# Kernel tuning notes

Measured on AMD Instinct MI355X. Metric: run time of the kernel, lower is better.

The kernel has to match this reference:

```python
import jax, jax.numpy as jnp
import numpy as np

B, L, E, H = 2, 2048, 1024, 16
D = E // H  # 64


def setup_inputs() -> dict:
    key = jax.random.key(0)
    ks = jax.random.split(key, 9)
    return {
        "query": jax.random.normal(ks[0], (B, L, E), dtype=jnp.float32),
        "value": jax.random.normal(ks[1], (B, L, E), dtype=jnp.float32),
        "key": jax.random.normal(ks[2], (B, L, E), dtype=jnp.float32),
        "mask": jax.random.randint(ks[3], (B, 1, L, L), 0, 2, dtype=jnp.int32),
        "Wq": jax.random.normal(ks[4], (D, D), dtype=jnp.float32) * 0.05,
        "Wk": jax.random.normal(ks[5], (D, D), dtype=jnp.float32) * 0.05,
        "Wv": jax.random.normal(ks[6], (D, D), dtype=jnp.float32) * 0.05,
        "Wfc": jax.random.normal(ks[7], (E, E), dtype=jnp.float32) * 0.02,
        "bfc": jax.random.normal(ks[8], (E,), dtype=jnp.float32) * 0.02,
    }


def reference(query, value, key, mask, Wq, Wk, Wv, Wfc, bfc):
    b, q_len, _ = query.shape
    k_len = key.shape[1]
    v_len = value.shape[1]
    # split heads: [b, l, H, D]
    q = query.reshape(b, q_len, H, D)
    k = key.reshape(b, k_len, H, D)
    v = value.reshape(b, v_len, H, D)
    # per-head linear projections (shared weights across heads, no bias)
    q = jnp.einsum('bqhd,ed->bqhe', q, Wq)
    k = jnp.einsum('bkhd,ed->bkhe', k, Wk)
    v = jnp.einsum('bvhd,ed->bvhe', v, Wv)
    # attention scores [b, H, q, k]
    attn = jnp.einsum('bqhd,bkhd->bhqk', q, k)
    # NOTE: original masks BEFORE scaling, and scales by sqrt(embedding_size)
    attn = jnp.where(mask == 0, jnp.float32(-1e20), attn)
    attn = attn / jnp.float32(E ** 0.5)
    attn = jax.nn.softmax(attn, axis=3)
    out = jnp.einsum('bhqk,bkhd->bqhd', attn, v).reshape(b, q_len, E)
    out = out @ Wfc.T + bfc
    return out
```

## Files before the change

kernel.cpp:

```cpp
#include <hip/hip_runtime.h>
#include <hip/hip_bf16.h>


#define B_ 2
#define L_ 2048
#define E_ 1024
#define H_ 16
#define D_ 64

typedef __attribute__((ext_vector_type(8))) short s8v;
typedef __attribute__((ext_vector_type(4))) float f4v;
typedef __attribute__((ext_vector_type(2))) float f2v;

__device__ __forceinline__ f4v mfma16(s8v a, s8v b, f4v c) {
    return __builtin_amdgcn_mfma_f32_16x16x32_bf16(a, b, c, 0, 0, 0);
}

__device__ __forceinline__ float fast_exp2(float x) {
    return __builtin_amdgcn_exp2f(x);
}

__device__ __forceinline__ ushort bf16bits(float f) {
    __hip_bfloat16 h = __float2bfloat16(f);
    return *(ushort*)&h;
}

__device__ __forceinline__ void glds16(const __hip_bfloat16* g, ushort* l) {
    __builtin_amdgcn_global_load_lds(
        (const __attribute__((address_space(1))) void*)g,
        (__attribute__((address_space(3))) void*)l,
        16, 0, 0);
}

__device__ __forceinline__ s8v ld8_dual(const void* p, size_t idx, bool isf32) {
    if (isf32) {
        const float* pf = (const float*)p + idx;
        f4v f0 = *(const f4v*)pf;
        f4v f1 = *(const f4v*)(pf + 4);
        s8v r;
        r[0] = (short)bf16bits(f0[0]); r[1] = (short)bf16bits(f0[1]);
        r[2] = (short)bf16bits(f0[2]); r[3] = (short)bf16bits(f0[3]);
        r[4] = (short)bf16bits(f1[0]); r[5] = (short)bf16bits(f1[1]);
        r[6] = (short)bf16bits(f1[2]); r[7] = (short)bf16bits(f1[3]);
        return r;
    }
    return *(const s8v*)((const __hip_bfloat16*)p + idx);
}

__device__ __forceinline__ s8v ld8_ws(const __hip_bfloat16* p) {
    return *(const s8v*)p;
}

__device__ __forceinline__ s8v u4_to_s8(uint a, uint b, uint c, uint d) {
    union { uint u[4]; s8v v; } x;
    x.u[0] = a; x.u[1] = b; x.u[2] = c; x.u[3] = d;
    return x.v;
}

__device__ __forceinline__ bool block_detect_f32(const void* q_in, int* sflag) {
    if (threadIdx.x == 0) *sflag = 0;
    __syncthreads();
    const ushort* qq = (const ushort*)q_in + (threadIdx.x & 255) * 16;
    int bad = 0;
    #pragma unroll
    for (int i = 0; i < 16; ++i) bad += (((qq[i] >> 7) & 0xFF) >= 0x8E);
    bad += __shfl_xor(bad, 1);
    bad += __shfl_xor(bad, 2);
    bad += __shfl_xor(bad, 4);
    bad += __shfl_xor(bad, 8);
    bad += __shfl_xor(bad, 16);
    bad += __shfl_xor(bad, 32);
    if ((threadIdx.x & 63) == 0 && threadIdx.x < 256) atomicAdd(sflag, bad);
    __syncthreads();
    return *sflag > 100;
}

__device__ __forceinline__ void cvt_piece(
    size_t i4, const void* Wfc, const void* bfc,
    __hip_bfloat16* wfc_bf, __hip_bfloat16* bfc_bf, bool isf32)
{
    const size_t base = i4 * 4;
    const size_t n1 = (size_t)E_ * E_;
    if (base >= n1 + E_) return;
    const void* src = (base < n1) ? Wfc : bfc;
    const size_t off = (base < n1) ? base : base - n1;
    __hip_bfloat16* dst = (base < n1) ? (wfc_bf + off) : (bfc_bf + off);
    if (isf32) {
        f4v v = *(const f4v*)((const float*)src + off);
        #pragma unroll
        for (int j = 0; j < 4; ++j) dst[j] = __float2bfloat16(v[j]);
    } else {
        *(ushort4*)dst = *(const ushort4*)((const ushort*)src + off);
    }
}

__global__ __launch_bounds__(256) void proj_all_kernel(
    const void* __restrict__ q_in, const void* __restrict__ k_in,
    const void* __restrict__ v_in,
    const void* __restrict__ Wq, const void* __restrict__ Wk,
    const void* __restrict__ Wv,
    const void* __restrict__ Wfc, const void* __restrict__ bfc,
    const int* __restrict__ mask, unsigned long long* __restrict__ mbits,
    __hip_bfloat16* __restrict__ qp, __hip_bfloat16* __restrict__ kp,
    __hip_bfloat16* __restrict__ vpT,
    __hip_bfloat16* __restrict__ wfc_bf, __hip_bfloat16* __restrict__ bfc_bf)
{
    __shared__ __align__(16) ushort tile[64][72];
    __shared__ __align__(16) ushort wlds[64 * 72];
    __shared__ int sflag;
    const int wave = threadIdx.x >> 6;
    const int lane = threadIdx.x & 63;
    const int quad = lane >> 4;
    const int l16  = lane & 15;

    if (blockIdx.y == 3) {
        const int lane_ = threadIdx.x & 63;
        const size_t wbase = (size_t)blockIdx.x * 128 + wave * 32;
        #pragma unroll 4
        for (int i = 0; i < 32; ++i) {
            const size_t widx = wbase + i;
            const int v = mask[widx * 64 + lane_];
            const unsigned long long bal = __ballot(v != 0);
            if (lane_ == 0) mbits[widx] = bal;
        }
        return;
    }

    const bool isf32 = block_detect_f32(q_in, &sflag);

    if (blockIdx.y == 4) {
        cvt_piece((size_t)blockIdx.x * 256 + threadIdx.x, Wfc, bfc, wfc_bf, bfc_bf, isf32);
        if (blockIdx.x == 0)
            cvt_piece((size_t)(E_ * (size_t)E_ / 4) + threadIdx.x, Wfc, bfc, wfc_bf, bfc_bf, isf32);
        return;
    }

    {
        const void* W = blockIdx.y == 0 ? Wq : (blockIdx.y == 1 ? Wk : Wv);
        const int row = threadIdx.x >> 2;
        const int c0  = (threadIdx.x & 3) * 16;
        if (isf32) {
            const float* wsrc = (const float*)W + row * 64 + c0;
            #pragma unroll
            for (int j = 0; j < 16; ++j)
                wlds[row * 72 + c0 + j] = bf16bits(wsrc[j]);
        } else {
            const ushort* wsrc = (const ushort*)W + row * 64 + c0;
            *(s8v*)&wlds[row * 72 + c0]     = *(const s8v*)wsrc;
            *(s8v*)&wlds[row * 72 + c0 + 8] = *(const s8v*)(wsrc + 8);
        }
    }
    __syncthreads();

    if (blockIdx.y < 2) {
        const void* X = blockIdx.y == 0 ? q_in : k_in;
        __hip_bfloat16* dst = blockIdx.y == 0 ? qp : kp;
        const float oscale = (blockIdx.y == 0) ? 0.045084439755930314f : 1.0f;
        const int m0 = (blockIdx.x * 4 + wave) * 16;

        const size_t abase = (size_t)(m0 + l16) * D_;
        s8v a0 = ld8_dual(X, abase + quad * 8, isf32);
        s8v a1 = ld8_dual(X, abase + 32 + quad * 8, isf32);

        f4v acc[4];
        #pragma unroll
        for (int nt = 0; nt < 4; ++nt) {
            const ushort* wr = &wlds[(nt * 16 + l16) * 72];
            s8v b0 = *(const s8v*)(wr + quad * 8);
            s8v b1 = *(const s8v*)(wr + 32 + quad * 8);
            f4v c = {0.f, 0.f, 0.f, 0.f};
            c = mfma16(a0, b0, c);
            c = mfma16(a1, b1, c);
            acc[nt] = c;
        }
        #pragma unroll
        for (int r = 0; r < 4; ++r) {
            const int m = m0 + quad * 4 + r;
            const int h = m & 15;
            const int bl = m >> 4;
            const int b = bl >> 11;
            const int l = bl & (L_ - 1);
            #pragma unroll
            for (int nt = 0; nt < 4; ++nt) {
                const int e = nt * 16 + l16;
                dst[(((size_t)(b * H_ + h)) * L_ + l) * D_ + e] =
                    __float2bfloat16(acc[nt][r] * oscale);
            }
        }
    } else {
        const int l0 = (blockIdx.x & 31) * 64;
        const int bh = blockIdx.x >> 5;
        const int b = bh >> 4, h = bh & 15;
        const int lw = l0 + wave * 16;

        const size_t xbase = ((size_t)(b * L_ + lw + l16)) * E_ + h * D_;
        s8v a0 = ld8_dual(v_in, xbase + quad * 8, isf32);
        s8v a1 = ld8_dual(v_in, xbase + 32 + quad * 8, isf32);

        #pragma unroll
        for (int nt = 0; nt < 4; ++nt) {
            const int e = nt * 16 + l16;
            const ushort* wr = &wlds[e * 72];
            s8v b0 = *(const s8v*)(wr + quad * 8);
            s8v b1 = *(const s8v*)(wr + 32 + quad * 8);
            f4v c = {0.f, 0.f, 0.f, 0.f};
            c = mfma16(a0, b0, c);
            c = mfma16(a1, b1, c);
            #pragma unroll
            for (int r = 0; r < 4; ++r)
                tile[wave * 16 + quad * 4 + r][e] = bf16bits(c[r]);
        }
        __syncthreads();
        const int e  = threadIdx.x >> 2;
        const int lc = (threadIdx.x & 3) * 16;
        s8v s0, s1;
        #pragma unroll
        for (int i = 0; i < 8; ++i) {
            s0[i] = (short)tile[lc + i][e];
            s1[i] = (short)tile[lc + 8 + i][e];
        }
        __hip_bfloat16* drow = vpT + ((size_t)bh * D_ + e) * L_ + l0 + lc;
        *(s8v*)drow = s0;
        *(s8v*)(drow + 8) = s1;
    }
}

__global__ __launch_bounds__(256) void cvt_wfc_kernel(
    const void* __restrict__ Wfc, const void* __restrict__ bfc,
    __hip_bfloat16* __restrict__ wfc_bf, __hip_bfloat16* __restrict__ bfc_bf,
    const void* __restrict__ q_in)
{
    __shared__ int sflag;
    const bool isf32 = block_detect_f32(q_in, &sflag);
    cvt_piece((size_t)blockIdx.x * 256 + threadIdx.x, Wfc, bfc, wfc_bf, bfc_bf, isf32);
}

__global__ __launch_bounds__(256, 2) void attn_kernel(
    const __hip_bfloat16* __restrict__ qp,
    const __hip_bfloat16* __restrict__ kp,
    const __hip_bfloat16* __restrict__ vpT,
    const unsigned long long* __restrict__ mbits,
    __hip_bfloat16* __restrict__ attn_out)
{
    __shared__ __align__(16) ushort kv[4][2][64 * 64];

    const int wave = threadIdx.x >> 6;
    const int lane = threadIdx.x & 63;
    const int quad = lane >> 4;
    const int l16  = lane & 15;
    const int sw   = l16 & 7;
    const int bh = blockIdx.y;
    const int b = bh >> 4, h = bh & 15;
    const int q0 = blockIdx.x * 128 + wave * 32;

    const __hip_bfloat16* kbh = kp + (size_t)bh * L_ * D_;
    const __hip_bfloat16* vbh = vpT + (size_t)bh * D_ * L_;
    const unsigned long long* mrowA = mbits + ((size_t)b * L_ + q0 + l16) * 32;
    const unsigned long long* mrowB = mrowA + 16 * 32;

    const int lrow = lane >> 3;
    const int lchk = (lane & 7) ^ lrow;
    const int r0 = wave * 16;
    const __hip_bfloat16* kg0 = kbh + (size_t)(r0 + lrow) * D_ + lchk * 8;
    const __hip_bfloat16* kg1 = kbh + (size_t)(r0 + 8 + lrow) * D_ + lchk * 8;
    const __hip_bfloat16* vg0 = vbh + (size_t)(r0 + lrow) * L_ + lchk * 8;
    const __hip_bfloat16* vg1 = vbh + (size_t)(r0 + 8 + lrow) * L_ + lchk * 8;

    const __hip_bfloat16* qbase = qp + ((size_t)bh * L_ + q0) * D_;
    s8v qaA0 = ld8_ws(qbase + (size_t)l16 * D_ + quad * 8);
    s8v qaA1 = ld8_ws(qbase + (size_t)l16 * D_ + 32 + quad * 8);
    s8v qaB0 = ld8_ws(qbase + (size_t)(16 + l16) * D_ + quad * 8);
    s8v qaB1 = ld8_ws(qbase + (size_t)(16 + l16) * D_ + 32 + quad * 8);

    f2v rs2A = {0.f, 0.f}, rs2B = {0.f, 0.f};
    f4v oA[4], oB[4];
    #pragma unroll
    for (int nt = 0; nt < 4; ++nt) {
        oA[nt] = (f4v){0.f, 0.f, 0.f, 0.f};
        oB[nt] = (f4v){0.f, 0.f, 0.f, 0.f};
    }

    const int ro0 = l16 * 64 + ((quad ^ sw) << 3);
    const int ro1 = l16 * 64 + (((quad + 4) ^ sw) << 3);
    const int shq = quad * 4;

    unsigned long long wqA0 = 0, wqA1 = 0, wqA2 = 0, wqA3 = 0;
    unsigned long long wqB0 = 0, wqB1 = 0, wqB2 = 0, wqB3 = 0;

    glds16(kg0, &kv[0][0][r0 * 64]);
    glds16(kg1, &kv[0][0][r0 * 64 + 512]);
    glds16(vg0, &kv[0][1][r0 * 64]);
    glds16(vg1, &kv[0][1][r0 * 64 + 512]);
    wqA0 = mrowA[0]; wqB0 = mrowB[0];
    kg0 += 64 * D_; kg1 += 64 * D_; vg0 += 64; vg1 += 64;
    glds16(kg0, &kv[1][0][r0 * 64]);
    glds16(kg1, &kv[1][0][r0 * 64 + 512]);
    glds16(vg0, &kv[1][1][r0 * 64]);
    glds16(vg1, &kv[1][1][r0 * 64 + 512]);
    wqA1 = mrowA[1]; wqB1 = mrowB[1];
    kg0 += 64 * D_; kg1 += 64 * D_; vg0 += 64; vg1 += 64;

#define SM_T(SARR_, WLO_, WHI_, RS_, PA0_, PA1_)                               \
    {                                                                          \
        uint dw[4][2];                                                         \
        _Pragma("unroll")                                                      \
        for (int nt = 0; nt < 4; ++nt) {                                       \
            const uint hs = (nt & 2) ? WHI_ : WLO_;                            \
            float pr[4];                                                       \
            _Pragma("unroll")                                                  \
            for (int r = 0; r < 4; ++r) {                                      \
                const float p = fast_exp2(SARR_[nt][r]);                       \
                const int m = __builtin_amdgcn_sbfe((int)hs,                   \
                                  ((nt & 1) << 4) + r, 1);                     \
                pr[r] = __uint_as_float(__float_as_uint(p) & (uint)m);         \
            }                                                                  \
            RS_ += (f2v){pr[0], pr[1]};                                        \
            RS_ += (f2v){pr[2], pr[3]};                                        \
            asm("v_cvt_pk_bf16_f32 %0, %1, %2"                                 \
                : "=v"(dw[nt][0]) : "v"(pr[0]), "v"(pr[1]));                   \
            asm("v_cvt_pk_bf16_f32 %0, %1, %2"                                 \
                : "=v"(dw[nt][1]) : "v"(pr[2]), "v"(pr[3]));                   \
        }                                                                      \
        uint w00 = dw[0][0], w10 = dw[1][0];                                   \
        uint w01 = dw[0][1], w11 = dw[1][1];                                   \
        uint w20 = dw[2][0], w30 = dw[3][0];                                   \
        uint w21 = dw[2][1], w31 = dw[3][1];                                   \
        asm("v_permlane32_swap_b32 %0, %1" : "+v"(w00), "+v"(w10));            \
        asm("v_permlane16_swap_b32 %0, %1" : "+v"(w00), "+v"(w10));            \
        asm("v_permlane32_swap_b32 %0, %1" : "+v"(w01), "+v"(w11));            \
        asm("v_permlane16_swap_b32 %0, %1" : "+v"(w01), "+v"(w11));            \
        asm("v_permlane32_swap_b32 %0, %1" : "+v"(w20), "+v"(w30));            \
        asm("v_permlane16_swap_b32 %0, %1" : "+v"(w20), "+v"(w30));            \
        asm("v_permlane32_swap_b32 %0, %1" : "+v"(w21), "+v"(w31));            \
        asm("v_permlane16_swap_b32 %0, %1" : "+v"(w21), "+v"(w31));            \
        PA0_ = u4_to_s8(w00, w01, w10, w11);                                   \
        PA1_ = u4_to_s8(w20, w21, w30, w31);                                   \
    }

#define ATTN_BODY(IT_, CUR_, DST_, PRE_, VMASM_)                               \
    {                                                                          \
        if (PRE_) {                                                            \
            glds16(kg0, &kv[DST_][0][r0 * 64]);                                \
            glds16(kg1, &kv[DST_][0][r0 * 64 + 512]);                          \
            glds16(vg0, &kv[DST_][1][r0 * 64]);                                \
            glds16(vg1, &kv[DST_][1][r0 * 64 + 512]);                          \
            wqA##DST_ = mrowA[(IT_) + 2];                                      \
            wqB##DST_ = mrowB[(IT_) + 2];                                      \
            kg0 += 64 * D_; kg1 += 64 * D_; vg0 += 64; vg1 += 64;              \
        }                                                                      \
        asm volatile(VMASM_ ::: "memory");                                     \
        __builtin_amdgcn_s_barrier();                                          \
        __builtin_amdgcn_sched_barrier(0);                                     \
        const uint wloA = ((uint)wqA##CUR_) >> shq;                            \
        const uint whiA = ((uint)(wqA##CUR_ >> 32)) >> shq;                    \
        const uint wloB = ((uint)wqB##CUR_) >> shq;                            \
        const uint whiB = ((uint)(wqB##CUR_ >> 32)) >> shq;                    \
        f4v sA[4], sB[4];                                                      \
        __builtin_amdgcn_s_setprio(1);                                         \
        _Pragma("unroll")                                                      \
        for (int nt = 0; nt < 4; ++nt) {                                       \
            s8v kb0 = *(const s8v*)&kv[CUR_][0][nt * 1024 + ro0];              \
            s8v kb1 = *(const s8v*)&kv[CUR_][0][nt * 1024 + ro1];              \
            f4v cA = {0.f, 0.f, 0.f, 0.f};                                     \
            f4v cB = {0.f, 0.f, 0.f, 0.f};                                     \
            cA = mfma16(kb0, qaA0, cA);                                        \
            cA = mfma16(kb1, qaA1, cA);                                        \
            cB = mfma16(kb0, qaB0, cB);                                        \
            cB = mfma16(kb1, qaB1, cB);                                        \
            sA[nt] = cA; sB[nt] = cB;                                          \
        }                                                                      \
        __builtin_amdgcn_s_setprio(0);                                         \
        s8v paA0, paA1, paB0, paB1;                                            \
        SM_T(sA, wloA, whiA, rs2A, paA0, paA1)                                 \
        SM_T(sB, wloB, whiB, rs2B, paB0, paB1)                                 \
        __builtin_amdgcn_s_setprio(1);                                         \
        _Pragma("unroll")                                                      \
        for (int nt = 0; nt < 4; ++nt) {                                       \
            s8v vb0 = *(const s8v*)&kv[CUR_][1][nt * 1024 + ro0];              \
            s8v vb1 = *(const s8v*)&kv[CUR_][1][nt * 1024 + ro1];              \
            oA[nt] = mfma16(paA0, vb0, oA[nt]);                                \
            oA[nt] = mfma16(paA1, vb1, oA[nt]);                                \
            oB[nt] = mfma16(paB0, vb0, oB[nt]);                                \
            oB[nt] = mfma16(paB1, vb1, oB[nt]);                                \
        }                                                                      \
        __builtin_amdgcn_s_setprio(0);                                         \
    }

    for (int it4 = 0; it4 < 7; ++it4) {
        const int t = it4 * 4;
        ATTN_BODY(t,     0, 2, true, "s_waitcnt vmcnt(12)")
        ATTN_BODY(t + 1, 1, 3, true, "s_waitcnt vmcnt(12)")
        ATTN_BODY(t + 2, 2, 0, true, "s_waitcnt vmcnt(12)")
        ATTN_BODY(t + 3, 3, 1, true, "s_waitcnt vmcnt(12)")
    }
    ATTN_BODY(28, 0, 2, true,  "s_waitcnt vmcnt(12)")
    ATTN_BODY(29, 1, 3, true,  "s_waitcnt vmcnt(12)")
    ATTN_BODY(30, 2, 0, false, "s_waitcnt vmcnt(6)")
    ATTN_BODY(31, 3, 1, false, "s_waitcnt vmcnt(0)")
#undef ATTN_BODY
#undef SM_T

    float vA = rs2A[0] + rs2A[1];
    vA += __shfl_xor(vA, 16, 64);
    vA += __shfl_xor(vA, 32, 64);
    float vB = rs2B[0] + rs2B[1];
    vB += __shfl_xor(vB, 16, 64);
    vB += __shfl_xor(vB, 32, 64);
    #pragma unroll
    for (int r = 0; r < 4; ++r) {
        const int qrow = quad * 4 + r;
        const float liA = __shfl(vA, qrow, 64);
        const float invA = 1.0f / fmaxf(liA, 1e-30f);
        const float liB = __shfl(vB, qrow, 64);
        const float invB = 1.0f / fmaxf(liB, 1e-30f);
        const int rowA = q0 + qrow;
        const int rowB = q0 + 16 + qrow;
        #pragma unroll
        for (int nt = 0; nt < 4; ++nt) {
            const int d = nt * 16 + l16;
            attn_out[((size_t)(b * L_ + rowA)) * E_ + h * D_ + d] =
                __float2bfloat16(oA[nt][r] * invA);
            attn_out[((size_t)(b * L_ + rowB)) * E_ + h * D_ + d] =
                __float2bfloat16(oB[nt][r] * invB);
        }
    }
}

__global__ __launch_bounds__(256, 4) void fc_kernel(
    const __hip_bfloat16* __restrict__ x,
    const __hip_bfloat16* __restrict__ wfc_bf,
    const __hip_bfloat16* __restrict__ bfc_bf,
    void* __restrict__ out, const void* __restrict__ q_in)
{
    __shared__ __align__(16) ushort abuf[2][128 * 64];
    __shared__ __align__(16) ushort bbuf[2][64 * 64];
    __shared__ int sflag;
    const bool isf32 = block_detect_f32(q_in, &sflag);
    const int wave = threadIdx.x >> 6;
    const int lane = threadIdx.x & 63;
    const int quad = lane >> 4;
    const int l16  = lane & 15;
    const int sw   = l16 & 7;
    const int m0 = blockIdx.x * 128;
    const int n0 = blockIdx.y * 64;
    const int wr = wave >> 1;
    const int wc = wave & 1;

    const int lrow = lane >> 3;
    const int lchk = (lane & 7) ^ lrow;

    const __hip_bfloat16* ag[4];
    #pragma unroll
    for (int c = 0; c < 4; ++c)
        ag[c] = x + (size_t)(m0 + c * 32 + wave * 8 + lrow) * E_ + lchk * 8;
    const __hip_bfloat16* bg[2];
    #pragma unroll
    for (int c = 0; c < 2; ++c)
        bg[c] = wfc_bf + (size_t)(n0 + c * 32 + wave * 8 + lrow) * E_ + lchk * 8;

    f4v acc[4][2];
    #pragma unroll
    for (int fm = 0; fm < 4; ++fm)
        #pragma unroll
        for (int fn = 0; fn < 2; ++fn) acc[fm][fn] = (f4v){0.f, 0.f, 0.f, 0.f};

    #pragma unroll
    for (int c = 0; c < 4; ++c) glds16(ag[c], &abuf[0][(c * 32 + wave * 8) * 64]);
    #pragma unroll
    for (int c = 0; c < 2; ++c) glds16(bg[c], &bbuf[0][(c * 32 + wave * 8) * 64]);
    __syncthreads();

    int cur = 0;
    for (int it = 0; it < 16; ++it) {
        if (it < 15) {
            #pragma unroll
            for (int c = 0; c < 4; ++c)
                glds16(ag[c] + (it + 1) * 64, &abuf[cur ^ 1][(c * 32 + wave * 8) * 64]);
            #pragma unroll
            for (int c = 0; c < 2; ++c)
                glds16(bg[c] + (it + 1) * 64, &bbuf[cur ^ 1][(c * 32 + wave * 8) * 64]);
        }
        s8v a0[4], a1[4];
        #pragma unroll
        for (int fm = 0; fm < 4; ++fm) {
            const ushort* ar = &abuf[cur][(wr * 64 + fm * 16 + l16) * 64];
            a0[fm] = *(const s8v*)(ar + ((quad ^ sw) << 3));
            a1[fm] = *(const s8v*)(ar + (((quad + 4) ^ sw) << 3));
        }
        #pragma unroll
        for (int fn = 0; fn < 2; ++fn) {
            const ushort* br = &bbuf[cur][(wc * 32 + fn * 16 + l16) * 64];
            s8v b0 = *(const s8v*)(br + ((quad ^ sw) << 3));
            s8v b1 = *(const s8v*)(br + (((quad + 4) ^ sw) << 3));
            #pragma unroll
            for (int fm = 0; fm < 4; ++fm) {
                acc[fm][fn] = mfma16(a0[fm], b0, acc[fm][fn]);
                acc[fm][fn] = mfma16(a1[fm], b1, acc[fm][fn]);
            }
        }
        __syncthreads();
        cur ^= 1;
    }
    #pragma unroll
    for (int fm = 0; fm < 4; ++fm) {
        #pragma unroll
        for (int r = 0; r < 4; ++r) {
            const int m = m0 + wr * 64 + fm * 16 + quad * 4 + r;
            #pragma unroll
            for (int fn = 0; fn < 2; ++fn) {
                const int n = n0 + wc * 32 + fn * 16 + l16;
                const float val = acc[fm][fn][r] + __bfloat162float(bfc_bf[n]);
                if (isf32) ((float*)out)[(size_t)m * E_ + n] = val;
                else       ((__hip_bfloat16*)out)[(size_t)m * E_ + n] = __float2bfloat16(val);
            }
        }
    }
}

extern "C" void kernel_launch(void* const* d_in, const int* in_sizes, int n_in,
                              void* d_out, int out_size, void* d_ws, size_t ws_size,
                              hipStream_t stream) {
    const void* query = d_in[0];
    const void* value = d_in[1];
    const void* key   = d_in[2];
    const int*  mask  = (const int*)d_in[3];
    const void* Wq  = d_in[4];
    const void* Wk  = d_in[5];
    const void* Wv  = d_in[6];
    const void* Wfc = d_in[7];
    const void* bfc = d_in[8];

    char* ws = (char*)d_ws;
    unsigned long long* mbits     = (unsigned long long*)(ws + (64u << 10));
    __hip_bfloat16* qp            = (__hip_bfloat16*)(ws + (2u  << 20));
    __hip_bfloat16* kp            = (__hip_bfloat16*)(ws + (10u << 20));
    __hip_bfloat16* vpT           = (__hip_bfloat16*)(ws + (18u << 20));
    __hip_bfloat16* attn_out      = (__hip_bfloat16*)(ws + (26u << 20));

    const bool big_ws = ws_size >= (37ull << 20);
    __hip_bfloat16* wfc_bf = big_ws ? (__hip_bfloat16*)(ws + (34ull << 20)) : qp;
    __hip_bfloat16* bfc_bf = wfc_bf + (size_t)E_ * E_;

    proj_all_kernel<<<dim3(1024, big_ws ? 5 : 4), 256, 0, stream>>>(
        query, key, value, Wq, Wk, Wv, Wfc, bfc, mask, mbits,
        qp, kp, vpT, wfc_bf, bfc_bf);
    attn_kernel<<<dim3(16, 32), 256, 0, stream>>>(qp, kp, vpT, mbits, attn_out);
    if (!big_ws)
        cvt_wfc_kernel<<<1025, 256, 0, stream>>>(Wfc, bfc, wfc_bf, bfc_bf, query);
    fc_kernel<<<dim3(32, 16), 256, 0, stream>>>(attn_out, wfc_bf, bfc_bf, d_out, query);
}
```

Before: 221.0 us.

## Double attention workgroup to 8 waves sharing each K/V LDS tile

Each attention workgroup now runs 8 waves covering 256 query rows instead of 4 waves covering 128, with half as many blocks. Every wave loads 8 rows of each K/V tile instead of 16, so each staged tile is reused by twice as many query rows and global K/V traffic per query row halves. The vmcnt wait thresholds drop to match the smaller per-wave load count. The trade-offs are more waves waiting at each barrier and a grid of 256 blocks, which may underfill the GPU's compute units.

```diff
diff --git a/kernel.cpp b/kernel.cpp
--- a/kernel.cpp
+++ b/kernel.cpp
@@ -235,7 +235,7 @@
     cvt_piece((size_t)blockIdx.x * 256 + threadIdx.x, Wfc, bfc, wfc_bf, bfc_bf, isf32);
 }
 
-__global__ __launch_bounds__(256, 2) void attn_kernel(
+__global__ __launch_bounds__(512, 2) void attn_kernel(
     const __hip_bfloat16* __restrict__ qp,
     const __hip_bfloat16* __restrict__ kp,
     const __hip_bfloat16* __restrict__ vpT,
@@ -251,7 +251,7 @@
     const int sw   = l16 & 7;
     const int bh = blockIdx.y;
     const int b = bh >> 4, h = bh & 15;
-    const int q0 = blockIdx.x * 128 + wave * 32;
+    const int q0 = blockIdx.x * 256 + wave * 32;
 
     const __hip_bfloat16* kbh = kp + (size_t)bh * L_ * D_;
     const __hip_bfloat16* vbh = vpT + (size_t)bh * D_ * L_;
@@ -260,11 +260,9 @@
 
     const int lrow = lane >> 3;
     const int lchk = (lane & 7) ^ lrow;
-    const int r0 = wave * 16;
-    const __hip_bfloat16* kg0 = kbh + (size_t)(r0 + lrow) * D_ + lchk * 8;
-    const __hip_bfloat16* kg1 = kbh + (size_t)(r0 + 8 + lrow) * D_ + lchk * 8;
-    const __hip_bfloat16* vg0 = vbh + (size_t)(r0 + lrow) * L_ + lchk * 8;
-    const __hip_bfloat16* vg1 = vbh + (size_t)(r0 + 8 + lrow) * L_ + lchk * 8;
+    const int r0 = wave * 8;
+    const __hip_bfloat16* kg = kbh + (size_t)(r0 + lrow) * D_ + lchk * 8;
+    const __hip_bfloat16* vg = vbh + (size_t)(r0 + lrow) * L_ + lchk * 8;
 
     const __hip_bfloat16* qbase = qp + ((size_t)bh * L_ + q0) * D_;
     s8v qaA0 = ld8_ws(qbase + (size_t)l16 * D_ + quad * 8);
@@ -287,18 +285,14 @@
     unsigned long long wqA0 = 0, wqA1 = 0, wqA2 = 0, wqA3 = 0;
     unsigned long long wqB0 = 0, wqB1 = 0, wqB2 = 0, wqB3 = 0;
 
-    glds16(kg0, &kv[0][0][r0 * 64]);
-    glds16(kg1, &kv[0][0][r0 * 64 + 512]);
-    glds16(vg0, &kv[0][1][r0 * 64]);
-    glds16(vg1, &kv[0][1][r0 * 64 + 512]);
+    glds16(kg, &kv[0][0][r0 * 64]);
+    glds16(vg, &kv[0][1][r0 * 64]);
     wqA0 = mrowA[0]; wqB0 = mrowB[0];
-    kg0 += 64 * D_; kg1 += 64 * D_; vg0 += 64; vg1 += 64;
-    glds16(kg0, &kv[1][0][r0 * 64]);
-    glds16(kg1, &kv[1][0][r0 * 64 + 512]);
-    glds16(vg0, &kv[1][1][r0 * 64]);
-    glds16(vg1, &kv[1][1][r0 * 64 + 512]);
+    kg += 64 * D_; vg += 64;
+    glds16(kg, &kv[1][0][r0 * 64]);
+    glds16(vg, &kv[1][1][r0 * 64]);
     wqA1 = mrowA[1]; wqB1 = mrowB[1];
-    kg0 += 64 * D_; kg1 += 64 * D_; vg0 += 64; vg1 += 64;
+    kg += 64 * D_; vg += 64;
 
 #define SM_T(SARR_, WLO_, WHI_, RS_, PA0_, PA1_)                               \
     {                                                                          \
@@ -340,13 +334,11 @@
 #define ATTN_BODY(IT_, CUR_, DST_, PRE_, VMASM_)                               \
     {                                                                          \
         if (PRE_) {                                                            \
-            glds16(kg0, &kv[DST_][0][r0 * 64]);                                \
-            glds16(kg1, &kv[DST_][0][r0 * 64 + 512]);                          \
-            glds16(vg0, &kv[DST_][1][r0 * 64]);                                \
-            glds16(vg1, &kv[DST_][1][r0 * 64 + 512]);                          \
+            glds16(kg, &kv[DST_][0][r0 * 64]);                                 \
+            glds16(vg, &kv[DST_][1][r0 * 64]);                                 \
             wqA##DST_ = mrowA[(IT_) + 2];                                      \
             wqB##DST_ = mrowB[(IT_) + 2];                                      \
-            kg0 += 64 * D_; kg1 += 64 * D_; vg0 += 64; vg1 += 64;              \
+            kg += 64 * D_; vg += 64;                                           \
         }                                                                      \
         asm volatile(VMASM_ ::: "memory");                                     \
         __builtin_amdgcn_s_barrier();                                          \
@@ -388,14 +380,14 @@
 
     for (int it4 = 0; it4 < 7; ++it4) {
         const int t = it4 * 4;
-        ATTN_BODY(t,     0, 2, true, "s_waitcnt vmcnt(12)")
-        ATTN_BODY(t + 1, 1, 3, true, "s_waitcnt vmcnt(12)")
-        ATTN_BODY(t + 2, 2, 0, true, "s_waitcnt vmcnt(12)")
-        ATTN_BODY(t + 3, 3, 1, true, "s_waitcnt vmcnt(12)")
-    }
-    ATTN_BODY(28, 0, 2, true,  "s_waitcnt vmcnt(12)")
-    ATTN_BODY(29, 1, 3, true,  "s_waitcnt vmcnt(12)")
-    ATTN_BODY(30, 2, 0, false, "s_waitcnt vmcnt(6)")
+        ATTN_BODY(t,     0, 2, true, "s_waitcnt vmcnt(8)")
+        ATTN_BODY(t + 1, 1, 3, true, "s_waitcnt vmcnt(8)")
+        ATTN_BODY(t + 2, 2, 0, true, "s_waitcnt vmcnt(8)")
+        ATTN_BODY(t + 3, 3, 1, true, "s_waitcnt vmcnt(8)")
+    }
+    ATTN_BODY(28, 0, 2, true,  "s_waitcnt vmcnt(8)")
+    ATTN_BODY(29, 1, 3, true,  "s_waitcnt vmcnt(8)")
+    ATTN_BODY(30, 2, 0, false, "s_waitcnt vmcnt(4)")
     ATTN_BODY(31, 3, 1, false, "s_waitcnt vmcnt(0)")
 #undef ATTN_BODY
 #undef SM_T
@@ -544,7 +536,7 @@
     proj_all_kernel<<<dim3(1024, big_ws ? 5 : 4), 256, 0, stream>>>(
         query, key, value, Wq, Wk, Wv, Wfc, bfc, mask, mbits,
         qp, kp, vpT, wfc_bf, bfc_bf);
-    attn_kernel<<<dim3(16, 32), 256, 0, stream>>>(qp, kp, vpT, mbits, attn_out);
+    attn_kernel<<<dim3(8, 32), 512, 0, stream>>>(qp, kp, vpT, mbits, attn_out);
     if (!big_ws)
         cvt_wfc_kernel<<<1025, 256, 0, stream>>>(Wfc, bfc, wfc_bf, bfc_bf, query);
     fc_kernel<<<dim3(32, 16), 256, 0, stream>>>(attn_out, wfc_bf, bfc_bf, d_out, query);
```

Result: faster. 214.4 us (-3.0%).
